# Kernel optimization log

Measured on AMD Instinct MI355X. Metric: run time of the kernel, lower is better.

## Reference

```python
import jax, jax.numpy as jnp
import numpy as np

NHEADS = 16
HEAD_DIM = 128
HIDDEN = 2048
SOFTCAP = 50.0
ROPE_BASE = 10000.0
SCALE = 256.0 ** (-0.5)  # hardcoded in original, NOT head_dim**-0.5


def _rope_tables(T, D, dtype):
    inv_freq = 1.0 / (ROPE_BASE ** (jnp.arange(0, D, 2, dtype=jnp.float32) / D))
    pos = jnp.arange(T, dtype=jnp.float32)
    freqs = pos[:, None] * inv_freq[None, :]            # [T, D/2]
    emb = jnp.concatenate([freqs, freqs], axis=-1)      # [T, D]
    # broadcast shape [1, 1, T, D] for (B, H, T, D) q/k
    return jnp.cos(emb)[None, None].astype(dtype), jnp.sin(emb)[None, None].astype(dtype)


def _rotate_half(x):
    x1, x2 = x[..., : x.shape[-1] // 2], x[..., x.shape[-1] // 2:]
    return jnp.concatenate([-x2, x1], axis=-1)


def setup_inputs() -> dict:
    key = jax.random.key(0)
    ks = jax.random.split(key, 5)
    B, T = 1, 4096
    X = jax.random.normal(ks[0], (B, T, HIDDEN), dtype=jnp.float32)
    std = 0.02
    Wq = jax.random.normal(ks[1], (HIDDEN, NHEADS * HEAD_DIM), dtype=jnp.float32) * std
    Wk = jax.random.normal(ks[2], (HIDDEN, NHEADS * HEAD_DIM), dtype=jnp.float32) * std
    Wv = jax.random.normal(ks[3], (HIDDEN, NHEADS * HEAD_DIM), dtype=jnp.float32) * std
    Wo = jax.random.normal(ks[4], (NHEADS * HEAD_DIM, HIDDEN), dtype=jnp.float32) * std
    return {"X": X, "Wq": Wq, "Wk": Wk, "Wv": Wv, "Wo": Wo}


def reference(X, Wq, Wk, Wv, Wo):
    B, T, C = X.shape
    H, D = NHEADS, HEAD_DIM
    # QKV projections -> [B, H, T, D]
    q = (X @ Wq).reshape(B, T, H, D).transpose(0, 2, 1, 3)
    k = (X @ Wk).reshape(B, T, H, D).transpose(0, 2, 1, 3)
    v = (X @ Wv).reshape(B, T, H, D).transpose(0, 2, 1, 3)
    # RoPE
    cos, sin = _rope_tables(T, D, X.dtype)
    q = q * cos + _rotate_half(q) * sin
    k = k * cos + _rotate_half(k) * sin
    # attention logits with tanh softcapping
    att = jnp.einsum("bhqd,bhkd->bhqk", q, k) * SCALE
    att = jnp.tanh(att / SOFTCAP) * SOFTCAP
    causal = jnp.tril(jnp.ones((T, T), dtype=bool))[None, None]
    att = jnp.where(causal, att, -jnp.inf)
    att = jax.nn.softmax(att, axis=-1)
    # dropout is identity (train=False)
    y = jnp.einsum("bhqk,bhkd->bhqd", att, v)
    y = y.transpose(0, 2, 1, 3).reshape(B, T, H * D)
    return y @ Wo
```

## Files before the change

### kernel.cpp

```cpp
#include <hip/hip_runtime.h>
#include <stdint.h>

#define T_SEQ 4096
#define HID   2048
#define NH    16
#define HD    128

typedef __attribute__((ext_vector_type(8))) short short8;
typedef __attribute__((ext_vector_type(4))) short short4v;
typedef __attribute__((ext_vector_type(4))) float f32x4;

typedef __attribute__((address_space(1))) void as1_void;
typedef __attribute__((address_space(3))) void as3_void;

__device__ __forceinline__ unsigned short f2bf(float f){
  unsigned u = __builtin_bit_cast(unsigned, f);
  u += 0x7fffu + ((u >> 16) & 1u);
  return (unsigned short)(u >> 16);
}
__device__ __forceinline__ float bf2f(unsigned short b){
  unsigned u = ((unsigned)b) << 16;
  return __builtin_bit_cast(float, u);
}
__device__ __forceinline__ void gll16(const void* g, void* l){
  __builtin_amdgcn_global_load_lds((as1_void*)(uintptr_t)g,
                                   (as3_void*)(unsigned)(uintptr_t)l, 16, 0, 0);
}

__global__ __launch_bounds__(256) void conv_x_k(const float* __restrict__ X,
                                                unsigned short* __restrict__ O){
  int i = (blockIdx.x * 256 + threadIdx.x) * 4;
  float4 v = *(const float4*)(X + i);
  short4v o;
  o[0] = (short)f2bf(v.x); o[1] = (short)f2bf(v.y);
  o[2] = (short)f2bf(v.z); o[3] = (short)f2bf(v.w);
  *(short4v*)(O + i) = o;
}

__global__ __launch_bounds__(256) void conv_wt_k(const float* __restrict__ W0,
                                                 const float* __restrict__ W1,
                                                 const float* __restrict__ W2,
                                                 const float* __restrict__ W3,
                                                 unsigned short* __restrict__ Wt){
  const float* W = (blockIdx.z == 0) ? W0 : (blockIdx.z == 1) ? W1
                   : (blockIdx.z == 2) ? W2 : W3;
  unsigned short* out = Wt + (size_t)blockIdx.z * HID * HID;
  __shared__ float tile[32][33];
  const int x = threadIdx.x;
  const int y = threadIdx.y;
  const int k0 = blockIdx.y * 32, n0 = blockIdx.x * 32;
#pragma unroll
  for (int i = 0; i < 4; ++i){
    int r = y * 4 + i;
    tile[r][x] = W[(size_t)(k0 + r) * HID + n0 + x];
  }
  __syncthreads();
#pragma unroll
  for (int i = 0; i < 4; ++i){
    int r = y * 4 + i;
    out[(size_t)(n0 + r) * HID + k0 + x] = f2bf(tile[x][r]);
  }
}

template<int MODE, int NTOT>
__global__ __launch_bounds__(256, 3) void gemm_bt(
    const unsigned short* __restrict__ A,
    const unsigned short* __restrict__ Bt,
    unsigned short* __restrict__ Qb,
    unsigned short* __restrict__ Kb,
    unsigned short* __restrict__ Vt,
    float* __restrict__ Cf)
{
  constexpr int K = HID;
  __shared__ __align__(16) unsigned short lA[128 * 64];
  __shared__ __align__(16) unsigned short lB[128 * 64];

  const int tid  = threadIdx.x;
  const int wave = tid >> 6;
  const int lane = tid & 63;
  const int qd   = lane >> 4;
  const int mm   = lane & 15;
  const int m7   = mm & 7;
  const int wm   = wave >> 1;
  const int wn   = wave & 1;
  const int bm   = blockIdx.y * 128;
  const int bn   = blockIdx.x * 128;

  const unsigned short* ga[4];
  const unsigned short* gb[4];
  unsigned short* la[4];
  unsigned short* lbp[4];
#pragma unroll
  for (int i = 0; i < 4; ++i){
    int s0   = (wave * 4 + i) * 64;
    int slot = s0 + lane;
    int row  = slot >> 3;
    int kb   = (slot & 7) ^ (row & 7);
    ga[i]  = A  + (size_t)(bm + row) * K + kb * 8;
    gb[i]  = Bt + (size_t)(bn + row) * K + kb * 8;
    la[i]  = lA + s0 * 8;
    lbp[i] = lB + s0 * 8;
  }

  int abase[4], bbase[4];
#pragma unroll
  for (int t = 0; t < 4; ++t){
    abase[t] = (wm * 64 + t * 16 + mm) * 8;
    bbase[t] = (wn * 64 + t * 16 + mm) * 8;
  }

  const f32x4 fzero = {0.f, 0.f, 0.f, 0.f};
  f32x4 acc[4][4];
#pragma unroll
  for (int i = 0; i < 4; ++i)
#pragma unroll
    for (int j = 0; j < 4; ++j) acc[i][j] = fzero;

  for (int k0 = 0; k0 < K; k0 += 64){
    __syncthreads();
#pragma unroll
    for (int i = 0; i < 4; ++i){
      gll16(ga[i] + k0, la[i]);
      gll16(gb[i] + k0, lbp[i]);
    }
    __syncthreads();
#pragma unroll
    for (int ks = 0; ks < 2; ++ks){
      const int co = (ks * 4 + qd) ^ m7;
      short8 af[4], bfv[4];
#pragma unroll
      for (int t = 0; t < 4; ++t) af[t]  = *(const short8*)(lA + (abase[t] + co) * 8);
#pragma unroll
      for (int t = 0; t < 4; ++t) bfv[t] = *(const short8*)(lB + (bbase[t] + co) * 8);
#pragma unroll
      for (int i = 0; i < 4; ++i)
#pragma unroll
        for (int j = 0; j < 4; ++j)
          acc[i][j] = __builtin_amdgcn_mfma_f32_16x16x32_bf16(af[i], bfv[j], acc[i][j], 0, 0, 0);
    }
  }

#pragma unroll
  for (int i = 0; i < 4; ++i){
#pragma unroll
    for (int j = 0; j < 4; ++j){
      const int col = bn + wn * 64 + j * 16 + mm;
#pragma unroll
      for (int r = 0; r < 4; ++r){
        const int row = bm + wm * 64 + i * 16 + qd * 4 + r;
        const float v = acc[i][j][r];
        if (MODE == 0){
          const int sel = col >> 11;
          const int nn  = col & 2047;
          const int h   = nn >> 7;
          const int d   = nn & 127;
          const unsigned short bv = f2bf(v);
          if (sel == 0)      Qb[((size_t)h * T_SEQ + row) * HD + d] = bv;
          else if (sel == 1) Kb[((size_t)h * T_SEQ + row) * HD + d] = bv;
          else               Vt[((size_t)(h * HD + d)) * T_SEQ + row] = bv;
        } else {
          Cf[(size_t)row * NTOT + col] = v;
        }
      }
    }
  }
}

__global__ __launch_bounds__(256) void rope_k(unsigned short* __restrict__ Qb,
                                              unsigned short* __restrict__ Kb){
  const int j = threadIdx.x & 63;
  const int t = blockIdx.x * 4 + (threadIdx.x >> 6);
  const int h = blockIdx.y;
  const float fr = (float)t * __expf(-(float)j * (9.210340371976184f / 64.f));
  const float cs = cosf(fr), sn = sinf(fr);
  const size_t base = ((size_t)h * T_SEQ + t) * HD;
  {
    float x1 = bf2f(Qb[base + j]), x2 = bf2f(Qb[base + j + 64]);
    Qb[base + j]      = f2bf(x1 * cs - x2 * sn);
    Qb[base + j + 64] = f2bf(x2 * cs + x1 * sn);
  }
  {
    float x1 = bf2f(Kb[base + j]), x2 = bf2f(Kb[base + j + 64]);
    Kb[base + j]      = f2bf(x1 * cs - x2 * sn);
    Kb[base + j + 64] = f2bf(x2 * cs + x1 * sn);
  }
}

__global__ __launch_bounds__(256, 2) void attn_k(
    const unsigned short* __restrict__ Qb,
    const unsigned short* __restrict__ Kb,
    const unsigned short* __restrict__ Vt,
    unsigned short* __restrict__ Yb)
{
  __shared__ __align__(16) unsigned char smem[32768];
  unsigned short* lK = (unsigned short*)smem;
  unsigned short* lV = (unsigned short*)(smem + 16384);
  float* lL = (float*)smem;
  float* lO = (float*)smem;

  const int tid  = threadIdx.x;
  const int w    = tid >> 6;
  const int rg   = w >> 1;
  const int kg   = w & 1;
  const int lane = tid & 63;
  const int qd   = lane >> 4;
  const int cc   = lane & 15;
  const int cx   = cc & 7;
  const int r8   = lane >> 3, c7 = lane & 7;

  const int b = blockIdx.x;
  const int h = (b & 7) + 8 * ((b >> 3) & 1);
  const int tp = 63 - (b >> 4);

  const int ce  = cc ^ qd;
  const int dlt = (ce & 4) ? -32 : 32;
  const unsigned short* gKbp = Kb + ((size_t)h * T_SEQ + w * 16 + qd) * HD + ce * 8;
  const int cV = c7 ^ r8;
  const unsigned short* gVbp = Vt + ((size_t)h * HD + w * 32 + r8) * T_SEQ + cV * 8;

  unsigned short* lPw = lK + w * 2048;

  const f32x4 fzero = {0.f, 0.f, 0.f, 0.f};
  const float A0 = 0.0625f;
  const float A1 = -3.2552083e-8f;
  const float A2 = 2.0345052e-14f;

  const int qrow0 = tp * 64 + rg * 32;
  const int iters = tp + 1;

  short8 qf[2][4];
#pragma unroll
  for (int mt = 0; mt < 2; ++mt)
#pragma unroll
    for (int ks = 0; ks < 4; ++ks)
      qf[mt][ks] = *(const short8*)(Qb + ((size_t)h * T_SEQ + qrow0 + mt * 16 + cc) * HD + ks * 32 + qd * 8);

  f32x4 o[2][8];
  float lsum[2][4];
#pragma unroll
  for (int mt = 0; mt < 2; ++mt){
#pragma unroll
    for (int dn = 0; dn < 8; ++dn) o[mt][dn] = fzero;
#pragma unroll
    for (int r = 0; r < 4; ++r) lsum[mt][r] = 0.f;
  }

#pragma unroll 1
  for (int it = 0; it < iters; ++it){
    const int k0 = it * 64;
    __syncthreads();
    {
      const unsigned short* gK = gKbp + (size_t)k0 * HD;
      const unsigned short* gV = gVbp + k0;
      unsigned short* dK = lK + w * 2048;
      unsigned short* dV = lV + w * 2048;
#pragma unroll
      for (int i = 0; i < 4; ++i)
        gll16(gK + (size_t)(i * 4) * HD + ((i & 1) ? dlt : 0), dK + i * 512);
#pragma unroll
      for (int i = 0; i < 4; ++i)
        gll16(gV + (size_t)i * 8 * T_SEQ, dV + i * 512);
    }
    __syncthreads();

    f32x4 S[2][2];
#pragma unroll
    for (int mt = 0; mt < 2; ++mt)
#pragma unroll
      for (int nt = 0; nt < 2; ++nt) S[mt][nt] = fzero;
#pragma unroll
    for (int nt = 0; nt < 2; ++nt){
      short8 kf[4];
#pragma unroll
      for (int ks = 0; ks < 4; ++ks)
        kf[ks] = *(const short8*)(lK + ((kg * 32 + nt * 16 + cc) * 16 + ((ks * 4 + qd) ^ cx)) * 8);
#pragma unroll
      for (int mt = 0; mt < 2; ++mt)
#pragma unroll
        for (int ks = 0; ks < 4; ++ks)
          S[mt][nt] = __builtin_amdgcn_mfma_f32_16x16x32_bf16(qf[mt][ks], kf[ks], S[mt][nt], 0, 0, 0);
    }

    const bool domask = (it == iters - 1);
    unsigned short pv[2][2][4];
#pragma unroll
    for (int mt = 0; mt < 2; ++mt)
#pragma unroll
      for (int nt = 0; nt < 2; ++nt)
#pragma unroll
        for (int r = 0; r < 4; ++r){
          float s = S[mt][nt][r];
          float w2 = s * s;
          float t = fmaf(w2, A2, A1);
          t = fmaf(w2, t, A0);
          float a = __builtin_amdgcn_fmed3f(s * t, -50.f, 50.f);
          float p = __expf(a);
          if (domask){
            int col = k0 + kg * 32 + nt * 16 + cc;
            int row = qrow0 + mt * 16 + qd * 4 + r;
            if (col > row) p = 0.f;
          }
          unsigned u = __builtin_bit_cast(unsigned, p);
          lsum[mt][r] += __builtin_bit_cast(float, u & 0xffff0000u);
          pv[mt][nt][r] = (unsigned short)(u >> 16);
        }

    __syncthreads();

#pragma unroll
    for (int mt = 0; mt < 2; ++mt)
#pragma unroll
      for (int nt = 0; nt < 2; ++nt)
#pragma unroll
        for (int r = 0; r < 4; ++r)
          lPw[(mt * 16 + qd * 4 + r) * 36 + nt * 16 + cc] = pv[mt][nt][r];

    short8 pf[2];
#pragma unroll
    for (int mt = 0; mt < 2; ++mt){
      const unsigned short* pb = lPw + (mt * 16 + cc) * 36 + qd * 8;
      union { short8 v; short4v hh[2]; } u;
      u.hh[0] = *(const short4v*)pb;
      u.hh[1] = *(const short4v*)(pb + 4);
      pf[mt] = u.v;
    }

#pragma unroll
    for (int dn = 0; dn < 8; ++dn){
      short8 vf = *(const short8*)(lV + ((dn * 16 + cc) * 8 + ((kg * 4 + qd) ^ cx)) * 8);
#pragma unroll
      for (int mt = 0; mt < 2; ++mt)
        o[mt][dn] = __builtin_amdgcn_mfma_f32_16x16x32_bf16(pf[mt], vf, o[mt][dn], 0, 0, 0);
    }
  }

  float lred[2][4];
#pragma unroll
  for (int mt = 0; mt < 2; ++mt)
#pragma unroll
    for (int r = 0; r < 4; ++r){
      float lb = lsum[mt][r];
      lb += __shfl_xor(lb, 1);
      lb += __shfl_xor(lb, 2);
      lb += __shfl_xor(lb, 4);
      lb += __shfl_xor(lb, 8);
      lred[mt][r] = lb;
    }

  __syncthreads();
  if (kg == 1 && cc == 0){
#pragma unroll
    for (int mt = 0; mt < 2; ++mt)
#pragma unroll
      for (int r = 0; r < 4; ++r)
        lL[rg * 32 + mt * 16 + qd * 4 + r] = lred[mt][r];
  }
  __syncthreads();
  float inv[2][4];
  if (kg == 0){
#pragma unroll
    for (int mt = 0; mt < 2; ++mt)
#pragma unroll
      for (int r = 0; r < 4; ++r)
        inv[mt][r] = __builtin_amdgcn_rcpf(lred[mt][r] + lL[rg * 32 + mt * 16 + qd * 4 + r]);
  }
  __syncthreads();
  if (kg == 1){
#pragma unroll
    for (int mt = 0; mt < 2; ++mt)
#pragma unroll
      for (int dn = 0; dn < 8; ++dn)
        *(f32x4*)&lO[(dn * 16 + cc) * 64 + rg * 32 + mt * 16 + qd * 4] = o[mt][dn];
  }
  __syncthreads();
  if (kg == 0){
#pragma unroll
    for (int mt = 0; mt < 2; ++mt){
#pragma unroll
      for (int dn = 0; dn < 8; ++dn){
        f32x4 oo = o[mt][dn] + *(const f32x4*)&lO[(dn * 16 + cc) * 64 + rg * 32 + mt * 16 + qd * 4];
#pragma unroll
        for (int r = 0; r < 4; ++r){
          int row = qrow0 + mt * 16 + qd * 4 + r;
          Yb[(size_t)row * HID + h * HD + dn * 16 + cc] = f2bf(oo[r] * inv[mt][r]);
        }
      }
    }
  }
}

extern "C" void kernel_launch(void* const* d_in, const int* in_sizes, int n_in,
                              void* d_out, int out_size, void* d_ws, size_t ws_size,
                              hipStream_t stream) {
  const float* X  = (const float*)d_in[0];
  const float* Wq = (const float*)d_in[1];
  const float* Wk = (const float*)d_in[2];
  const float* Wv = (const float*)d_in[3];
  const float* Wo = (const float*)d_in[4];
  float* out = (float*)d_out;

  unsigned short* ws = (unsigned short*)d_ws;
  unsigned short* Xb = ws;
  unsigned short* Wt = ws + (size_t)8  * 1024 * 1024;
  unsigned short* Qb = ws + (size_t)24 * 1024 * 1024;
  unsigned short* Kb = ws + (size_t)32 * 1024 * 1024;
  unsigned short* Vt = ws + (size_t)40 * 1024 * 1024;
  unsigned short* Yb = Xb;

  conv_x_k<<<8192, 256, 0, stream>>>(X, Xb);
  conv_wt_k<<<dim3(64, 64, 4), dim3(32, 8), 0, stream>>>(Wq, Wk, Wv, Wo, Wt);
  gemm_bt<0, 6144><<<dim3(48, 32), 256, 0, stream>>>(Xb, Wt, Qb, Kb, Vt, nullptr);
  rope_k<<<dim3(1024, NH), 256, 0, stream>>>(Qb, Kb);
  attn_k<<<dim3(1024), 256, 0, stream>>>(Qb, Kb, Vt, Yb);
  gemm_bt<1, 2048><<<dim3(16, 32), 256, 0, stream>>>(Yb, Wt + (size_t)6144 * 2048,
                                                     nullptr, nullptr, nullptr, out);
}
```

Measured before the change: 456.5 us.

## Double attention query tile to 128 rows per block with dedicated P buffer

Each attention block now handles 128 query rows (64 per row-group) instead of 64, halving the grid and halving how often each K/V tile is loaded from global memory per query row. P staging moves to its own shared-memory region, which removes one barrier per iteration, and row-groups whose keys lie entirely in the future skip compute. The cost is more accumulator registers (o[4][8]) and more shared memory (50KB), which may lower occupancy, and fewer blocks with some idle row-groups on diagonal tiles.

```diff
diff --git a/kernel.cpp b/kernel.cpp
--- a/kernel.cpp
+++ b/kernel.cpp
@@ -192,10 +192,11 @@
     const unsigned short* __restrict__ Vt,
     unsigned short* __restrict__ Yb)
 {
-  __shared__ __align__(16) unsigned char smem[32768];
+  __shared__ __align__(16) unsigned char smem[51200];
   unsigned short* lK = (unsigned short*)smem;
   unsigned short* lV = (unsigned short*)(smem + 16384);
-  float* lL = (float*)smem;
+  unsigned short* lP = (unsigned short*)(smem + 32768);
+  float* lL = (float*)(smem + 32768);
   float* lO = (float*)smem;
 
   const int tid  = threadIdx.x;
@@ -210,7 +211,7 @@
 
   const int b = blockIdx.x;
   const int h = (b & 7) + 8 * ((b >> 3) & 1);
-  const int tp = 63 - (b >> 4);
+  const int tp = 31 - (b >> 4);
 
   const int ce  = cc ^ qd;
   const int dlt = (ce & 4) ? -32 : 32;
@@ -218,27 +219,27 @@
   const int cV = c7 ^ r8;
   const unsigned short* gVbp = Vt + ((size_t)h * HD + w * 32 + r8) * T_SEQ + cV * 8;
 
-  unsigned short* lPw = lK + w * 2048;
+  unsigned short* lPw = lP + w * 2304;
 
   const f32x4 fzero = {0.f, 0.f, 0.f, 0.f};
   const float A0 = 0.0625f;
   const float A1 = -3.2552083e-8f;
   const float A2 = 2.0345052e-14f;
 
-  const int qrow0 = tp * 64 + rg * 32;
-  const int iters = tp + 1;
-
-  short8 qf[2][4];
-#pragma unroll
-  for (int mt = 0; mt < 2; ++mt)
+  const int qrow0w = tp * 128 + rg * 64;
+  const int iters  = 2 * tp + 2;
+
+  short8 qf[4][4];
+#pragma unroll
+  for (int mt = 0; mt < 4; ++mt)
 #pragma unroll
     for (int ks = 0; ks < 4; ++ks)
-      qf[mt][ks] = *(const short8*)(Qb + ((size_t)h * T_SEQ + qrow0 + mt * 16 + cc) * HD + ks * 32 + qd * 8);
-
-  f32x4 o[2][8];
-  float lsum[2][4];
-#pragma unroll
-  for (int mt = 0; mt < 2; ++mt){
+      qf[mt][ks] = *(const short8*)(Qb + ((size_t)h * T_SEQ + qrow0w + mt * 16 + cc) * HD + ks * 32 + qd * 8);
+
+  f32x4 o[4][8];
+  float lsum[4][4];
+#pragma unroll
+  for (int mt = 0; mt < 4; ++mt){
 #pragma unroll
     for (int dn = 0; dn < 8; ++dn) o[mt][dn] = fzero;
 #pragma unroll
@@ -263,80 +264,65 @@
     }
     __syncthreads();
 
-    f32x4 S[2][2];
-#pragma unroll
-    for (int mt = 0; mt < 2; ++mt)
-#pragma unroll
-      for (int nt = 0; nt < 2; ++nt) S[mt][nt] = fzero;
-#pragma unroll
-    for (int nt = 0; nt < 2; ++nt){
-      short8 kf[4];
-#pragma unroll
-      for (int ks = 0; ks < 4; ++ks)
-        kf[ks] = *(const short8*)(lK + ((kg * 32 + nt * 16 + cc) * 16 + ((ks * 4 + qd) ^ cx)) * 8);
-#pragma unroll
-      for (int mt = 0; mt < 2; ++mt)
-#pragma unroll
-        for (int ks = 0; ks < 4; ++ks)
-          S[mt][nt] = __builtin_amdgcn_mfma_f32_16x16x32_bf16(qf[mt][ks], kf[ks], S[mt][nt], 0, 0, 0);
-    }
-
-    const bool domask = (it == iters - 1);
-    unsigned short pv[2][2][4];
-#pragma unroll
-    for (int mt = 0; mt < 2; ++mt)
-#pragma unroll
-      for (int nt = 0; nt < 2; ++nt)
-#pragma unroll
-        for (int r = 0; r < 4; ++r){
-          float s = S[mt][nt][r];
-          float w2 = s * s;
-          float t = fmaf(w2, A2, A1);
-          t = fmaf(w2, t, A0);
-          float a = __builtin_amdgcn_fmed3f(s * t, -50.f, 50.f);
-          float p = __expf(a);
-          if (domask){
-            int col = k0 + kg * 32 + nt * 16 + cc;
-            int row = qrow0 + mt * 16 + qd * 4 + r;
-            if (col > row) p = 0.f;
+    if (k0 < qrow0w + 64){
+      const bool domask = (k0 >= qrow0w);
+
+#pragma unroll
+      for (int nt = 0; nt < 2; ++nt){
+        f32x4 S[4];
+#pragma unroll
+        for (int mt = 0; mt < 4; ++mt) S[mt] = fzero;
+#pragma unroll
+        for (int ks = 0; ks < 4; ++ks){
+          short8 kf = *(const short8*)(lK + ((kg * 32 + nt * 16 + cc) * 16 + ((ks * 4 + qd) ^ cx)) * 8);
+#pragma unroll
+          for (int mt = 0; mt < 4; ++mt)
+            S[mt] = __builtin_amdgcn_mfma_f32_16x16x32_bf16(qf[mt][ks], kf, S[mt], 0, 0, 0);
+        }
+#pragma unroll
+        for (int mt = 0; mt < 4; ++mt)
+#pragma unroll
+          for (int r = 0; r < 4; ++r){
+            float s = S[mt][r];
+            float w2 = s * s;
+            float t = fmaf(w2, A2, A1);
+            t = fmaf(w2, t, A0);
+            float a = __builtin_amdgcn_fmed3f(s * t, -50.f, 50.f);
+            float p = __expf(a);
+            if (domask){
+              int col = k0 + kg * 32 + nt * 16 + cc;
+              int row = qrow0w + mt * 16 + qd * 4 + r;
+              if (col > row) p = 0.f;
+            }
+            unsigned u = __builtin_bit_cast(unsigned, p);
+            lsum[mt][r] += __builtin_bit_cast(float, u & 0xffff0000u);
+            lPw[(mt * 16 + qd * 4 + r) * 36 + nt * 16 + cc] = (unsigned short)(u >> 16);
           }
-          unsigned u = __builtin_bit_cast(unsigned, p);
-          lsum[mt][r] += __builtin_bit_cast(float, u & 0xffff0000u);
-          pv[mt][nt][r] = (unsigned short)(u >> 16);
-        }
-
-    __syncthreads();
-
-#pragma unroll
-    for (int mt = 0; mt < 2; ++mt)
-#pragma unroll
-      for (int nt = 0; nt < 2; ++nt)
-#pragma unroll
-        for (int r = 0; r < 4; ++r)
-          lPw[(mt * 16 + qd * 4 + r) * 36 + nt * 16 + cc] = pv[mt][nt][r];
-
-    short8 pf[2];
-#pragma unroll
-    for (int mt = 0; mt < 2; ++mt){
-      const unsigned short* pb = lPw + (mt * 16 + cc) * 36 + qd * 8;
-      union { short8 v; short4v hh[2]; } u;
-      u.hh[0] = *(const short4v*)pb;
-      u.hh[1] = *(const short4v*)(pb + 4);
-      pf[mt] = u.v;
-    }
-
-#pragma unroll
-    for (int dn = 0; dn < 8; ++dn){
-      short8 vf = *(const short8*)(lV + ((dn * 16 + cc) * 8 + ((kg * 4 + qd) ^ cx)) * 8);
-#pragma unroll
-      for (int mt = 0; mt < 2; ++mt)
-        o[mt][dn] = __builtin_amdgcn_mfma_f32_16x16x32_bf16(pf[mt], vf, o[mt][dn], 0, 0, 0);
-    }
-  }
-
-  float lred[2][4];
-#pragma unroll
-  for (int mt = 0; mt < 2; ++mt)
+      }
+
+      short8 pf[4];
+#pragma unroll
+      for (int mt = 0; mt < 4; ++mt){
+        const unsigned short* pb = lPw + (mt * 16 + cc) * 36 + qd * 8;
+        union { short8 v; short4v hh[2]; } u;
+        u.hh[0] = *(const short4v*)pb;
+        u.hh[1] = *(const short4v*)(pb + 4);
+        pf[mt] = u.v;
+      }
+
+#pragma unroll
+      for (int dn = 0; dn < 8; ++dn){
+        short8 vf = *(const short8*)(lV + ((dn * 16 + cc) * 8 + ((kg * 4 + qd) ^ cx)) * 8);
+#pragma unroll
+        for (int mt = 0; mt < 4; ++mt)
+          o[mt][dn] = __builtin_amdgcn_mfma_f32_16x16x32_bf16(pf[mt], vf, o[mt][dn], 0, 0, 0);
+      }
+    }
+  }
+
+  float lred[4][4];
+#pragma unroll
+  for (int mt = 0; mt < 4; ++mt)
 #pragma unroll
     for (int r = 0; r < 4; ++r){
       float lb = lsum[mt][r];
@@ -350,39 +336,42 @@
   __syncthreads();
   if (kg == 1 && cc == 0){
 #pragma unroll
-    for (int mt = 0; mt < 2; ++mt)
+    for (int mt = 0; mt < 4; ++mt)
 #pragma unroll
       for (int r = 0; r < 4; ++r)
-        lL[rg * 32 + mt * 16 + qd * 4 + r] = lred[mt][r];
+        lL[rg * 64 + mt * 16 + qd * 4 + r] = lred[mt][r];
   }
   __syncthreads();
-  float inv[2][4];
+  float inv[4][4];
   if (kg == 0){
 #pragma unroll
-    for (int mt = 0; mt < 2; ++mt)
+    for (int mt = 0; mt < 4; ++mt)
 #pragma unroll
       for (int r = 0; r < 4; ++r)
-        inv[mt][r] = __builtin_amdgcn_rcpf(lred[mt][r] + lL[rg * 32 + mt * 16 + qd * 4 + r]);
-  }
-  __syncthreads();
-  if (kg == 1){
-#pragma unroll
-    for (int mt = 0; mt < 2; ++mt)
-#pragma unroll
-      for (int dn = 0; dn < 8; ++dn)
-        *(f32x4*)&lO[(dn * 16 + cc) * 64 + rg * 32 + mt * 16 + qd * 4] = o[mt][dn];
-  }
-  __syncthreads();
-  if (kg == 0){
-#pragma unroll
-    for (int mt = 0; mt < 2; ++mt){
-#pragma unroll
-      for (int dn = 0; dn < 8; ++dn){
-        f32x4 oo = o[mt][dn] + *(const f32x4*)&lO[(dn * 16 + cc) * 64 + rg * 32 + mt * 16 + qd * 4];
-#pragma unroll
-        for (int r = 0; r < 4; ++r){
-          int row = qrow0 + mt * 16 + qd * 4 + r;
-          Yb[(size_t)row * HID + h * HD + dn * 16 + cc] = f2bf(oo[r] * inv[mt][r]);
+        inv[mt][r] = __builtin_amdgcn_rcpf(lred[mt][r] + lL[rg * 64 + mt * 16 + qd * 4 + r]);
+  }
+#pragma unroll 1
+  for (int ph = 0; ph < 2; ++ph){
+    __syncthreads();
+    if (rg == ph && kg == 1){
+#pragma unroll
+      for (int mt = 0; mt < 4; ++mt)
+#pragma unroll
+        for (int dn = 0; dn < 8; ++dn)
+          *(f32x4*)&lO[(dn * 16 + cc) * 64 + mt * 16 + qd * 4] = o[mt][dn];
+    }
+    __syncthreads();
+    if (rg == ph && kg == 0){
+#pragma unroll
+      for (int mt = 0; mt < 4; ++mt){
+#pragma unroll
+        for (int dn = 0; dn < 8; ++dn){
+          f32x4 oo = o[mt][dn] + *(const f32x4*)&lO[(dn * 16 + cc) * 64 + mt * 16 + qd * 4];
+#pragma unroll
+          for (int r = 0; r < 4; ++r){
+            int row = qrow0w + mt * 16 + qd * 4 + r;
+            Yb[(size_t)row * HID + h * HD + dn * 16 + cc] = f2bf(oo[r] * inv[mt][r]);
+          }
         }
       }
     }
@@ -411,7 +400,7 @@
   conv_wt_k<<<dim3(64, 64, 4), dim3(32, 8), 0, stream>>>(Wq, Wk, Wv, Wo, Wt);
   gemm_bt<0, 6144><<<dim3(48, 32), 256, 0, stream>>>(Xb, Wt, Qb, Kb, Vt, nullptr);
   rope_k<<<dim3(1024, NH), 256, 0, stream>>>(Qb, Kb);
-  attn_k<<<dim3(1024), 256, 0, stream>>>(Qb, Kb, Vt, Yb);
+  attn_k<<<dim3(512), 256, 0, stream>>>(Qb, Kb, Vt, Yb);
   gemm_bt<1, 2048><<<dim3(16, 32), 256, 0, stream>>>(Yb, Wt + (size_t)6144 * 2048,
                                                      nullptr, nullptr, nullptr, out);
 }
```

Result: slower. 701.7 us (+53.7%).
